# Optimization experiments

Hardware: AMD Instinct MI355X
Metric: run time of the kernel (lower is better)

The kernel has to match this reference:

```python
import jax, jax.numpy as jnp
import numpy as np
import itertools

# LeViT-style Attention config (matches init_kwargs)
DIM = 256
KD = 32          # key_dim
H = 8            # num_heads
AR = 4           # attn_ratio
RES = 14
N = RES * RES    # 196 tokens
D = AR * KD      # per-head value dim = 128
DH = D * H       # 1024
NHKD = KD * H    # 256
HID = DH + 2 * NHKD  # 1536 = qkv width
EPS = 1e-5
SCALE = KD ** -0.5
BATCH = 256


def _bias_idxs():
    # Same construction as the torch module: index into table of unique abs offsets.
    points = list(itertools.product(range(RES), range(RES)))
    offs = {}
    idxs = []
    for p1 in points:
        for p2 in points:
            o = (abs(p1[0] - p2[0]), abs(p1[1] - p2[1]))
            if o not in offs:
                offs[o] = len(offs)
            idxs.append(offs[o])
    return np.asarray(idxs, dtype=np.int32).reshape(N, N), len(offs)


def _bn(x, g, b):
    # BatchNorm1d in training mode over the flattened (B*N, F) batch dim.
    mu = x.mean(axis=0)
    var = jnp.var(x, axis=0)  # biased, as torch BN uses for normalization
    return (x - mu) * jax.lax.rsqrt(var + EPS) * g + b


def setup_inputs() -> dict:
    key = jax.random.key(0)
    ks = jax.random.split(key, 8)
    idxs_np, n_off = _bias_idxs()  # n_off == 196 for RES=14
    x = jax.random.normal(ks[0], (BATCH, N, DIM), dtype=jnp.float32)
    Wqkv = jax.random.normal(ks[1], (HID, DIM), dtype=jnp.float32) * 0.02
    g1 = 1.0 + 0.1 * jax.random.normal(ks[2], (HID,), dtype=jnp.float32)
    b1 = 0.1 * jax.random.normal(ks[3], (HID,), dtype=jnp.float32)
    # init is zeros in the module; use small randn so the bias path is exercised
    bias_table = 0.1 * jax.random.normal(ks[4], (H, n_off), dtype=jnp.float32)
    Wproj = jax.random.normal(ks[5], (DIM, DH), dtype=jnp.float32) * 0.02
    # bn_weight_init=0 in module; use nonzero so output/grads are nontrivial
    g2 = 1.0 + 0.1 * jax.random.normal(ks[6], (DIM,), dtype=jnp.float32)
    b2 = 0.1 * jax.random.normal(ks[7], (DIM,), dtype=jnp.float32)
    return {
        "x": x, "Wqkv": Wqkv, "g1": g1, "b1": b1,
        "bias_table": bias_table, "Wproj": Wproj, "g2": g2, "b2": b2,
        "idxs": jnp.asarray(idxs_np),
    }


def reference(x, Wqkv, g1, b1, bias_table, Wproj, g2, b2, idxs):
    B, Ntok, C = x.shape
    # qkv = Linear_BN(x): bias-free linear then BN over flattened (B*N, HID)
    h = jnp.einsum('bnc,hc->bnh', x, Wqkv)
    h = _bn(h.reshape(B * Ntok, HID), g1, b1).reshape(B, Ntok, H, -1)
    q = h[..., :KD].transpose(0, 2, 1, 3)            # (B,H,N,KD)
    k = h[..., KD:2 * KD].transpose(0, 2, 1, 3)      # (B,H,N,KD)
    v = h[..., 2 * KD:].transpose(0, 2, 1, 3)        # (B,H,N,D)
    bias = bias_table[:, idxs]                       # (H,N,N) relative-position bias gather
    attn = jnp.einsum('bhnd,bhmd->bhnm', q, k) * SCALE + bias
    attn = jax.nn.softmax(attn, axis=-1)
    o = jnp.einsum('bhnm,bhmd->bhnd', attn, v)
    o = o.transpose(0, 2, 1, 3).reshape(B, Ntok, DH)
    # proj = Hardswish -> Linear_BN(dh, dim)
    o = o * jnp.clip(o + 3.0, 0.0, 6.0) / 6.0
    o = jnp.einsum('bnd,cd->bnc', o, Wproj)
    o = _bn(o.reshape(B * Ntok, C), g2, b2).reshape(B, Ntok, C)
    return o
```

## Files before the change

kernel.cpp:

```cpp
#include <hip/hip_runtime.h>

typedef _Float16 f16;
typedef __attribute__((ext_vector_type(8))) _Float16 half8;
typedef __attribute__((ext_vector_type(4))) _Float16 half4;
typedef __attribute__((ext_vector_type(4))) float   f4;

#define NTOK   196
#define MROWS  50176
#define HIDN   1536
#define HPC    192
#define DHD    1024
#define EPSV   1e-5f
#define SCALEV 0.17677669529663687f

#define GLD16(gp, lp) __builtin_amdgcn_global_load_lds( \
    (const __attribute__((address_space(1))) unsigned int*)(gp), \
    (__attribute__((address_space(3))) unsigned int*)(lp), 16, 0, 0)

__device__ inline int swz8(int row) { return (((row & 7) ^ ((row >> 3) & 7))) * 8; }

__global__ void cvt_f32_f16(const float* __restrict__ src, f16* __restrict__ dst, int n4)
{
    int i = blockIdx.x * blockDim.x + threadIdx.x;
    if (i < n4) {
        float4 v = *(const float4*)&src[i * 4];
        half4 h = { (f16)v.x, (f16)v.y, (f16)v.z, (f16)v.w };
        *(half4*)&dst[i * 4] = h;
    }
}

__global__ void build_bias(const float* __restrict__ bt, const int* __restrict__ idxs,
                           f16* __restrict__ bf)
{
    int i = blockIdx.x * 256 + threadIdx.x;
    if (i >= 8 * 208 * 224) return;
    int k = i % 224, q = (i / 224) % 208, h = i / (224 * 208);
    float v = -30000.f;
    if (q < NTOK && k < NTOK) v = bt[h * NTOK + idxs[q * NTOK + k]];
    bf[i] = (f16)v;
}

__global__ __launch_bounds__(256) void gemm1_qkv(
    const f16* __restrict__ A, const f16* __restrict__ B,
    f16* __restrict__ C, float* __restrict__ gsum, float* __restrict__ gsq)
{
    const int K = 256, ldc = HIDN;
    __shared__ f16 As[128 * 32];
    __shared__ f16 Bs[128 * 32];
    __shared__ float ssum[128], ssq[128];

    const int t = threadIdx.x;
    const int m0 = blockIdx.x * 128, n0 = blockIdx.y * 128;
    const int wid = t >> 6, lane = t & 63, quad = lane >> 4, lm = lane & 15;
    const int wm = (wid >> 1) * 64, wn = (wid & 1) * 64;

    const int lr = lane >> 2, lc = (lane & 3) * 8;
    f16* As0 = &As[(wid * 2 + 0) * 512];
    f16* As1 = &As[(wid * 2 + 1) * 512];
    f16* Bs0 = &Bs[(wid * 2 + 0) * 512];
    f16* Bs1 = &Bs[(wid * 2 + 1) * 512];
    const f16* Ab = A + (long)(m0 + wid * 32 + lr) * K + lc;
    const f16* Bb = B + (long)(n0 + wid * 32 + lr) * K + lc;

    f4 acc[4][4] = {};

    for (int k0 = 0; k0 < K; k0 += 32) {
        GLD16(Ab + k0,          As0);
        GLD16(Ab + 16 * K + k0, As1);
        GLD16(Bb + k0,          Bs0);
        GLD16(Bb + 16 * K + k0, Bs1);
        __syncthreads();
        half8 a[4], b[4];
        #pragma unroll
        for (int i = 0; i < 4; ++i) a[i] = *(const half8*)&As[(wm + i*16 + lm) * 32 + quad * 8];
        #pragma unroll
        for (int j = 0; j < 4; ++j) b[j] = *(const half8*)&Bs[(wn + j*16 + lm) * 32 + quad * 8];
        #pragma unroll
        for (int i = 0; i < 4; ++i)
            #pragma unroll
            for (int j = 0; j < 4; ++j)
                acc[i][j] = __builtin_amdgcn_mfma_f32_16x16x32_f16(a[i], b[j], acc[i][j], 0, 0, 0);
        __syncthreads();
    }

    if (t < 128) { ssum[t] = 0.f; ssq[t] = 0.f; }
    __syncthreads();

    #pragma unroll
    for (int j = 0; j < 4; ++j) {
        int nl = wn + j*16 + lm;
        float psum = 0.f, psq = 0.f;
        #pragma unroll
        for (int i = 0; i < 4; ++i) {
            #pragma unroll
            for (int r = 0; r < 4; ++r) {
                int ml = wm + i*16 + quad*4 + r;
                float v = acc[i][j][r];
                f16 uh = (f16)v;
                float vb = (float)uh;
                C[(long)(m0 + ml) * ldc + n0 + nl] = uh;
                psum += vb; psq += vb * vb;
            }
        }
        atomicAdd(&ssum[nl], psum);
        atomicAdd(&ssq[nl], psq);
    }
    __syncthreads();
    if (t < 128) {
        atomicAdd(&gsum[n0 + t], ssum[t]);
        atomicAdd(&gsq[n0 + t],  ssq[t]);
    }
}

__global__ __launch_bounds__(256) void gemm2_proj(
    const f16* __restrict__ A, const f16* __restrict__ B,
    float* __restrict__ C, float* __restrict__ gsum, float* __restrict__ gsq)
{
    const int K = 1024, ldc = 256;
    __shared__ f16 As[128 * 32];
    __shared__ f16 Bs[128 * 32];
    __shared__ float ssum[128], ssq[128];

    const int t = threadIdx.x;
    const int m0 = blockIdx.x * 128, n0 = blockIdx.y * 128;
    const int wid = t >> 6, lane = t & 63, quad = lane >> 4, lm = lane & 15;
    const int wm = (wid >> 1) * 64, wn = (wid & 1) * 64;

    const int lr = lane >> 2, lc = (lane & 3) * 8;
    f16* As0 = &As[(wid * 2 + 0) * 512];
    f16* As1 = &As[(wid * 2 + 1) * 512];
    f16* Bs0 = &Bs[(wid * 2 + 0) * 512];
    f16* Bs1 = &Bs[(wid * 2 + 1) * 512];
    const f16* Ab = A + (long)(m0 + wid * 32 + lr) * K + lc;
    const f16* Bb = B + (long)(n0 + wid * 32 + lr) * K + lc;

    f4 acc[4][4] = {};

    for (int k0 = 0; k0 < K; k0 += 32) {
        GLD16(Ab + k0,          As0);
        GLD16(Ab + 16 * K + k0, As1);
        GLD16(Bb + k0,          Bs0);
        GLD16(Bb + 16 * K + k0, Bs1);
        __syncthreads();
        half8 a[4], b[4];
        #pragma unroll
        for (int i = 0; i < 4; ++i) a[i] = *(const half8*)&As[(wm + i*16 + lm) * 32 + quad * 8];
        #pragma unroll
        for (int j = 0; j < 4; ++j) b[j] = *(const half8*)&Bs[(wn + j*16 + lm) * 32 + quad * 8];
        #pragma unroll
        for (int i = 0; i < 4; ++i)
            #pragma unroll
            for (int j = 0; j < 4; ++j)
                acc[i][j] = __builtin_amdgcn_mfma_f32_16x16x32_f16(a[i], b[j], acc[i][j], 0, 0, 0);
        __syncthreads();
    }

    if (t < 128) { ssum[t] = 0.f; ssq[t] = 0.f; }
    __syncthreads();

    #pragma unroll
    for (int j = 0; j < 4; ++j) {
        int nl = wn + j*16 + lm;
        float psum = 0.f, psq = 0.f;
        #pragma unroll
        for (int i = 0; i < 4; ++i) {
            #pragma unroll
            for (int r = 0; r < 4; ++r) {
                int ml = wm + i*16 + quad*4 + r;
                float v = acc[i][j][r];
                C[(long)(m0 + ml) * ldc + n0 + nl] = v;
                psum += v; psq += v * v;
            }
        }
        atomicAdd(&ssum[nl], psum);
        atomicAdd(&ssq[nl], psq);
    }
    __syncthreads();
    if (t < 128) {
        atomicAdd(&gsum[n0 + t], ssum[t]);
        atomicAdd(&gsq[n0 + t],  ssq[t]);
    }
}

__global__ void bn_fin(const float* __restrict__ gsum, const float* __restrict__ gsq,
                       const float* __restrict__ g, const float* __restrict__ b,
                       float* __restrict__ a_out, float* __restrict__ s_out, int nch)
{
    int c = blockIdx.x * blockDim.x + threadIdx.x;
    if (c >= nch) return;
    float inv  = 1.f / (float)MROWS;
    float mean = gsum[c] * inv;
    float var  = gsq[c] * inv - mean * mean;
    float a    = g[c] * rsqrtf(var + EPSV);
    a_out[c] = a;
    s_out[c] = b[c] - mean * a;
}

__global__ __launch_bounds__(832) void attn_kernel(
    const f16* __restrict__ hbuf, const float* __restrict__ a1, const float* __restrict__ s1,
    const f16* __restrict__ bf, f16* __restrict__ obuf)
{
    __shared__ f16   ks[208][32];
    __shared__ f16   vT[128][256];
    __shared__ float af[192], sf[192];

    const int t  = threadIdx.x;
    const int bb = blockIdx.x >> 3;
    const int hh = blockIdx.x & 7;
    const int wid = t >> 6, lane = t & 63, quad = lane >> 4, lm = lane & 15;

    if (t < 192) { af[t] = a1[hh * HPC + t]; sf[t] = s1[hh * HPC + t]; }
    half8 z8 = {};
    for (int i = t; i < 4096; i += 832) *(half8*)&vT[i >> 5][(i & 31) * 8] = z8;
    if (t < 384) ks[196 + (t >> 5)][t & 31] = (f16)0.f;
    __syncthreads();

    {
        int t8 = t & 7;
        for (int rr = t >> 3; rr < NTOK; rr += 104) {
            const f16* hrow = hbuf + (long)(bb * NTOK + rr) * HIDN + hh * HPC;
            int sr = swz8(rr);
            #pragma unroll
            for (int cc = 0; cc < 3; ++cc) {
                int cb = 32 + (t8 + cc * 8) * 8;
                if (cb >= 192) continue;
                half8 raw = *(const half8*)(hrow + cb);
                if (cb < 64) {
                    half8 ov;
                    #pragma unroll
                    for (int e = 0; e < 8; ++e)
                        ov[e] = (f16)((float)raw[e] * af[cb + e] + sf[cb + e]);
                    *(half8*)&ks[rr][(cb - 32 + sr) & 31] = ov;
                } else {
                    #pragma unroll
                    for (int e = 0; e < 8; ++e) {
                        int c = cb - 64 + e;
                        f16 ov = (f16)((float)raw[e] * af[cb + e] + sf[cb + e]);
                        vT[c][(rr + swz8(c)) & 255] = ov;
                    }
                }
            }
        }
    }
    __syncthreads();

    const int mt = wid;
    const int qrow = mt * 16 + lm;
    const f16* bfh = bf + hh * 208 * 224;

    long grow = (long)bb * NTOK + qrow;
    if (grow > (long)(MROWS - 1)) grow = MROWS - 1;
    half8 qraw = *(const half8*)(hbuf + grow * HIDN + hh * HPC + quad * 8);
    half8 qf;
    #pragma unroll
    for (int e = 0; e < 8; ++e)
        qf[e] = (f16)((float)qraw[e] * af[quad * 8 + e] + sf[quad * 8 + e]);

    f4 sreg[13];
    #pragma unroll
    for (int nt = 0; nt < 13; ++nt) {
        int krow = nt * 16 + lm;
        half8 ak = *(const half8*)&ks[krow][(quad * 8 + swz8(krow)) & 31];
        f4 z = {};
        sreg[nt] = __builtin_amdgcn_mfma_f32_16x16x32_f16(ak, qf, z, 0, 0, 0);
    }

    const f16* brow = bfh + qrow * 224 + quad * 4;
    float m = -3.0e38f;
    #pragma unroll
    for (int nt = 0; nt < 13; ++nt) {
        half4 b4 = *(const half4*)(brow + nt * 16);
        #pragma unroll
        for (int r = 0; r < 4; ++r) {
            sreg[nt][r] = fmaf(sreg[nt][r], SCALEV, (float)b4[r]);
            m = fmaxf(m, sreg[nt][r]);
        }
    }
    m = fmaxf(m, __shfl_xor(m, 16));
    m = fmaxf(m, __shfl_xor(m, 32));

    float s = 0.f;
    half4 ap[13];
    #pragma unroll
    for (int nt = 0; nt < 13; ++nt) {
        float e0 = __expf(sreg[nt][0] - m);
        float e1 = __expf(sreg[nt][1] - m);
        float e2 = __expf(sreg[nt][2] - m);
        float e3 = __expf(sreg[nt][3] - m);
        s += (e0 + e1) + (e2 + e3);
        ap[nt] = half4{ (f16)e0, (f16)e1, (f16)e2, (f16)e3 };
    }
    s += __shfl_xor(s, 16);
    s += __shfl_xor(s, 32);
    float rinv = 1.f / s;

    float rv[4];
    #pragma unroll
    for (int r = 0; r < 4; ++r) rv[r] = __shfl(rinv, quad * 4 + r);

    #pragma unroll
    for (int ct = 0; ct < 8; ++ct) {
        int c = ct * 16 + lm;
        int sc = swz8(c);
        f4 oa = {};
        #pragma unroll
        for (int nt = 0; nt < 13; ++nt) {
            half4 bv = *(const half4*)&vT[c][(nt * 16 + quad * 4 + sc) & 255];
            oa = __builtin_amdgcn_mfma_f32_16x16x16f16(ap[nt], bv, oa, 0, 0, 0);
        }
        #pragma unroll
        for (int r = 0; r < 4; ++r) {
            int qr = mt * 16 + quad * 4 + r;
            if (qr < 196) {
                float v  = oa[r] * rv[r];
                float hs = v * fminf(fmaxf(v + 3.f, 0.f), 6.f) * (1.f / 6.f);
                obuf[(long)(bb * NTOK + qr) * DHD + hh * 128 + c] = (f16)hs;
            }
        }
    }
}

__global__ __launch_bounds__(256) void bn_apply(
    float* __restrict__ out, const float* __restrict__ a2, const float* __restrict__ s2)
{
    __shared__ float aL[256], sL[256];
    int t = threadIdx.x;
    aL[t] = a2[t]; sL[t] = s2[t];
    __syncthreads();
    long total = (long)MROWS * 256 / 4;
    for (long i = (long)blockIdx.x * 256 + t; i < total; i += (long)gridDim.x * 256) {
        float4 v = *(float4*)&out[i * 4];
        int cb = (int)((i * 4) & 255);
        v.x = v.x * aL[cb + 0] + sL[cb + 0];
        v.y = v.y * aL[cb + 1] + sL[cb + 1];
        v.z = v.z * aL[cb + 2] + sL[cb + 2];
        v.w = v.w * aL[cb + 3] + sL[cb + 3];
        *(float4*)&out[i * 4] = v;
    }
}

extern "C" void kernel_launch(void* const* d_in, const int* in_sizes, int n_in,
                              void* d_out, int out_size, void* d_ws, size_t ws_size,
                              hipStream_t stream)
{
    (void)in_sizes; (void)n_in; (void)out_size; (void)ws_size;
    const float* x          = (const float*)d_in[0];
    const float* Wqkv       = (const float*)d_in[1];
    const float* g1         = (const float*)d_in[2];
    const float* b1         = (const float*)d_in[3];
    const float* bias_table = (const float*)d_in[4];
    const float* Wproj      = (const float*)d_in[5];
    const float* g2         = (const float*)d_in[6];
    const float* b2         = (const float*)d_in[7];
    const int*   idxs       = (const int*)d_in[8];
    float*       out        = (float*)d_out;

    char* ws = (char*)d_ws;
    f16* hbuf = (f16*)ws;
    f16* obuf = (f16*)(ws + 154140672LL);
    f16* xh   = (f16*)(ws + 154140672LL);
    f16* wqh  = (f16*)(ws + 154140672LL + 25690112LL);
    f16* wph  = (f16*)ws;
    float* stats = (float*)(ws + 256901120LL);
    float* gsum1 = stats;            float* gsq1 = stats + 1536;
    float* gsum2 = stats + 3072;     float* gsq2 = stats + 3328;
    float* a1 = stats + 3584;        float* s1 = a1 + 1536;
    float* a2 = s1 + 1536;           float* s2 = a2 + 256;
    f16* bias_full = (f16*)(ws + 256901120LL + 65536LL);

    hipMemsetAsync(stats, 0, 3584 * sizeof(float), stream);

    cvt_f32_f16<<<12544, 256, 0, stream>>>(x, xh, 3211264);
    cvt_f32_f16<<<384,   256, 0, stream>>>(Wqkv, wqh, 98304);
    build_bias<<<1456, 256, 0, stream>>>(bias_table, idxs, bias_full);

    gemm1_qkv<<<dim3(392, 12), 256, 0, stream>>>(xh, wqh, hbuf, gsum1, gsq1);
    bn_fin<<<6, 256, 0, stream>>>(gsum1, gsq1, g1, b1, a1, s1, 1536);

    attn_kernel<<<2048, 832, 0, stream>>>(hbuf, a1, s1, bias_full, obuf);

    cvt_f32_f16<<<256, 256, 0, stream>>>(Wproj, wph, 65536);

    gemm2_proj<<<dim3(392, 2), 256, 0, stream>>>(obuf, wph, out, gsum2, gsq2);
    bn_fin<<<1, 256, 0, stream>>>(gsum2, gsq2, g2, b2, a2, s2, 256);

    bn_apply<<<1024, 256, 0, stream>>>(out, a2, s2);
}
```

Measured before the change: 449.2 us.

## Triple-buffer GEMM LDS tiles with async prefetch and XOR-swizzled layout

Rewrites the K loops of both GEMM kernels into a three-stage software pipeline. Global-to-LDS loads for stage k+2 are issued while stage k is computed, with one barrier per step and vmcnt gating in place of two full syncthreads. The LDS tile columns are XOR-swizzled to cut bank conflicts on the half8 fragment reads. The cost is triple the LDS footprint, which may lower occupancy, plus hand-written waitcnt logic that has to stay correct.

```diff
diff --git a/kernel.cpp b/kernel.cpp
--- a/kernel.cpp
+++ b/kernel.cpp
@@ -40,13 +40,42 @@
     bf[i] = (f16)v;
 }
 
+#define PIPE_BODY(CA, CB, PA, PB, ST, HASPF, GATE)                              \
+  {                                                                             \
+    asm volatile("s_waitcnt vmcnt(" GATE ")" ::: "memory");                     \
+    __builtin_amdgcn_s_barrier();                                               \
+    __builtin_amdgcn_sched_barrier(0);                                          \
+    if (HASPF) {                                                                \
+      const f16* Apf_ = Ab + ((ST) + 2) * 32;                                   \
+      const f16* Bpf_ = Bb + ((ST) + 2) * 32;                                   \
+      GLD16(Apf_,          &PA[so0]);                                           \
+      GLD16(Apf_ + 16 * K, &PA[so1]);                                           \
+      GLD16(Bpf_,          &PB[so0]);                                           \
+      GLD16(Bpf_ + 16 * K, &PB[so1]);                                           \
+    }                                                                           \
+    half8 a_[4], b_[4];                                                         \
+    _Pragma("unroll")                                                           \
+    for (int i_ = 0; i_ < 4; ++i_) {                                            \
+      a_[i_] = *(const half8*)&CA[(wm + i_ * 16 + lm) * 32 + rs];               \
+      b_[i_] = *(const half8*)&CB[(wn + i_ * 16 + lm) * 32 + rs];               \
+    }                                                                           \
+    asm volatile("s_waitcnt lgkmcnt(0)" ::: "memory");                          \
+    __builtin_amdgcn_sched_barrier(0);                                          \
+    _Pragma("unroll")                                                           \
+    for (int i_ = 0; i_ < 4; ++i_)                                              \
+      _Pragma("unroll")                                                         \
+      for (int j_ = 0; j_ < 4; ++j_)                                            \
+        acc[i_][j_] = __builtin_amdgcn_mfma_f32_16x16x32_f16(                   \
+            a_[i_], b_[j_], acc[i_][j_], 0, 0, 0);                              \
+  }
+
 __global__ __launch_bounds__(256) void gemm1_qkv(
     const f16* __restrict__ A, const f16* __restrict__ B,
     f16* __restrict__ C, float* __restrict__ gsum, float* __restrict__ gsq)
 {
     const int K = 256, ldc = HIDN;
-    __shared__ f16 As[128 * 32];
-    __shared__ f16 Bs[128 * 32];
+    __shared__ f16 As0[4096], As1[4096], As2[4096];
+    __shared__ f16 Bs0[4096], Bs1[4096], Bs2[4096];
     __shared__ float ssum[128], ssq[128];
 
     const int t = threadIdx.x;
@@ -54,35 +83,34 @@
     const int wid = t >> 6, lane = t & 63, quad = lane >> 4, lm = lane & 15;
     const int wm = (wid >> 1) * 64, wn = (wid & 1) * 64;
 
-    const int lr = lane >> 2, lc = (lane & 3) * 8;
-    f16* As0 = &As[(wid * 2 + 0) * 512];
-    f16* As1 = &As[(wid * 2 + 1) * 512];
-    f16* Bs0 = &Bs[(wid * 2 + 0) * 512];
-    f16* Bs1 = &Bs[(wid * 2 + 1) * 512];
+    const int lr = lane >> 2;
+    const int lc = ((lane & 3) ^ (lr & 3)) * 8;
+    const int so0 = (wid * 2 + 0) * 512, so1 = (wid * 2 + 1) * 512;
     const f16* Ab = A + (long)(m0 + wid * 32 + lr) * K + lc;
     const f16* Bb = B + (long)(n0 + wid * 32 + lr) * K + lc;
+    const int rs = (quad ^ (lm & 3)) * 8;
 
     f4 acc[4][4] = {};
 
-    for (int k0 = 0; k0 < K; k0 += 32) {
-        GLD16(Ab + k0,          As0);
-        GLD16(Ab + 16 * K + k0, As1);
-        GLD16(Bb + k0,          Bs0);
-        GLD16(Bb + 16 * K + k0, Bs1);
-        __syncthreads();
-        half8 a[4], b[4];
-        #pragma unroll
-        for (int i = 0; i < 4; ++i) a[i] = *(const half8*)&As[(wm + i*16 + lm) * 32 + quad * 8];
-        #pragma unroll
-        for (int j = 0; j < 4; ++j) b[j] = *(const half8*)&Bs[(wn + j*16 + lm) * 32 + quad * 8];
-        #pragma unroll
-        for (int i = 0; i < 4; ++i)
-            #pragma unroll
-            for (int j = 0; j < 4; ++j)
-                acc[i][j] = __builtin_amdgcn_mfma_f32_16x16x32_f16(a[i], b[j], acc[i][j], 0, 0, 0);
-        __syncthreads();
-    }
-
+    GLD16(Ab,               &As0[so0]);
+    GLD16(Ab + 16 * K,      &As0[so1]);
+    GLD16(Bb,               &Bs0[so0]);
+    GLD16(Bb + 16 * K,      &Bs0[so1]);
+    GLD16(Ab + 32,          &As1[so0]);
+    GLD16(Ab + 16 * K + 32, &As1[so1]);
+    GLD16(Bb + 32,          &Bs1[so0]);
+    GLD16(Bb + 16 * K + 32, &Bs1[so1]);
+
+    PIPE_BODY(As0, Bs0, As2, Bs2, 0, 1, "4");
+    PIPE_BODY(As1, Bs1, As0, Bs0, 1, 1, "4");
+    PIPE_BODY(As2, Bs2, As1, Bs1, 2, 1, "4");
+    PIPE_BODY(As0, Bs0, As2, Bs2, 3, 1, "4");
+    PIPE_BODY(As1, Bs1, As0, Bs0, 4, 1, "4");
+    PIPE_BODY(As2, Bs2, As1, Bs1, 5, 1, "4");
+    PIPE_BODY(As0, Bs0, As2, Bs2, 6, 0, "4");
+    PIPE_BODY(As1, Bs1, As0, Bs0, 7, 0, "0");
+
+    __syncthreads();
     if (t < 128) { ssum[t] = 0.f; ssq[t] = 0.f; }
     __syncthreads();
 
@@ -117,8 +145,8 @@
     float* __restrict__ C, float* __restrict__ gsum, float* __restrict__ gsq)
 {
     const int K = 1024, ldc = 256;
-    __shared__ f16 As[128 * 32];
-    __shared__ f16 Bs[128 * 32];
+    __shared__ f16 As0[4096], As1[4096], As2[4096];
+    __shared__ f16 Bs0[4096], Bs1[4096], Bs2[4096];
     __shared__ float ssum[128], ssq[128];
 
     const int t = threadIdx.x;
@@ -126,35 +154,36 @@
     const int wid = t >> 6, lane = t & 63, quad = lane >> 4, lm = lane & 15;
     const int wm = (wid >> 1) * 64, wn = (wid & 1) * 64;
 
-    const int lr = lane >> 2, lc = (lane & 3) * 8;
-    f16* As0 = &As[(wid * 2 + 0) * 512];
-    f16* As1 = &As[(wid * 2 + 1) * 512];
-    f16* Bs0 = &Bs[(wid * 2 + 0) * 512];
-    f16* Bs1 = &Bs[(wid * 2 + 1) * 512];
+    const int lr = lane >> 2;
+    const int lc = ((lane & 3) ^ (lr & 3)) * 8;
+    const int so0 = (wid * 2 + 0) * 512, so1 = (wid * 2 + 1) * 512;
     const f16* Ab = A + (long)(m0 + wid * 32 + lr) * K + lc;
     const f16* Bb = B + (long)(n0 + wid * 32 + lr) * K + lc;
+    const int rs = (quad ^ (lm & 3)) * 8;
 
     f4 acc[4][4] = {};
 
-    for (int k0 = 0; k0 < K; k0 += 32) {
-        GLD16(Ab + k0,          As0);
-        GLD16(Ab + 16 * K + k0, As1);
-        GLD16(Bb + k0,          Bs0);
-        GLD16(Bb + 16 * K + k0, Bs1);
-        __syncthreads();
-        half8 a[4], b[4];
-        #pragma unroll
-        for (int i = 0; i < 4; ++i) a[i] = *(const half8*)&As[(wm + i*16 + lm) * 32 + quad * 8];
-        #pragma unroll
-        for (int j = 0; j < 4; ++j) b[j] = *(const half8*)&Bs[(wn + j*16 + lm) * 32 + quad * 8];
-        #pragma unroll
-        for (int i = 0; i < 4; ++i)
-            #pragma unroll
-            for (int j = 0; j < 4; ++j)
-                acc[i][j] = __builtin_amdgcn_mfma_f32_16x16x32_f16(a[i], b[j], acc[i][j], 0, 0, 0);
-        __syncthreads();
-    }
-
+    GLD16(Ab,               &As0[so0]);
+    GLD16(Ab + 16 * K,      &As0[so1]);
+    GLD16(Bb,               &Bs0[so0]);
+    GLD16(Bb + 16 * K,      &Bs0[so1]);
+    GLD16(Ab + 32,          &As1[so0]);
+    GLD16(Ab + 16 * K + 32, &As1[so1]);
+    GLD16(Bb + 32,          &Bs1[so0]);
+    GLD16(Bb + 16 * K + 32, &Bs1[so1]);
+
+    for (int s = 0; s < 30; s += 6) {
+        PIPE_BODY(As0, Bs0, As2, Bs2, s + 0, 1, "4");
+        PIPE_BODY(As1, Bs1, As0, Bs0, s + 1, 1, "4");
+        PIPE_BODY(As2, Bs2, As1, Bs1, s + 2, 1, "4");
+        PIPE_BODY(As0, Bs0, As2, Bs2, s + 3, 1, "4");
+        PIPE_BODY(As1, Bs1, As0, Bs0, s + 4, 1, "4");
+        PIPE_BODY(As2, Bs2, As1, Bs1, s + 5, 1, "4");
+    }
+    PIPE_BODY(As0, Bs0, As2, Bs2, 30, 0, "4");
+    PIPE_BODY(As1, Bs1, As0, Bs0, 31, 0, "0");
+
+    __syncthreads();
     if (t < 128) { ssum[t] = 0.f; ssq[t] = 0.f; }
     __syncthreads();
 
```

New measurement: 440.9 us. About the same (-1.8%).
